# Performance work log

Measured on AMD Instinct MI355X. Metric: run time of the kernel, lower is better.

The kernel has to match this reference:

```python
import jax, jax.numpy as jnp
import numpy as np

B, H, Wd, CIN = 4, 64, 64, 65   # batch, height, width, in_channels (incl. time)
COUT = 256                      # out_channels (incl. time)
K = 3
KK = K * K
PAD, STRIDE = 1, 1
SOUT = 4                        # output_stabilizer_size (C4 rotations)
CURV = 1.0                      # Lorentz manifold curvature k
LIN_FEAT = (CIN - 1) * KK + 1   # 577


def make_c4_z2_indices(ksize):
    # (out_rotation, in_stabilizer=1, u, v, [s, u_src, v_src]) index table,
    # realizing the C4 filter rotation as a gather (as in GrouPy).
    f = np.arange(ksize * ksize).reshape(ksize, ksize)
    inds = np.zeros((4, 1, ksize, ksize, 3), dtype=np.int64)
    for r in range(4):
        rot = np.rot90(f, r)
        u, v = np.unravel_index(rot, (ksize, ksize))
        inds[r, 0, :, :, 1] = u
        inds[r, 0, :, :, 2] = v
    return inds

INDS = make_c4_z2_indices(K)


def setup_inputs() -> dict:
    key = jax.random.key(0)
    k1, k2, k3 = jax.random.split(key, 3)
    stdv = float(np.sqrt(2.0 / ((CIN - 1) * KK)))  # reset_parameters
    x = jax.random.normal(k1, (B, H, Wd, CIN), dtype=jnp.float32)
    W = jax.random.uniform(k2, (COUT, LIN_FEAT), minval=-stdv, maxval=stdv, dtype=jnp.float32)
    b = jax.random.uniform(k3, (COUT,), minval=-stdv, maxval=stdv, dtype=jnp.float32)
    return {"x": x, "W": W, "b": b}


def _unfold(x):
    # x: (B, C, H, W) -> (B, C*KK, Ho*Wo) in torch.nn.Unfold layout (channel-major, kernel-minor)
    xp = jnp.pad(x, ((0, 0), (0, 0), (PAD, PAD), (PAD, PAD)))
    ho = (H + 2 * PAD - K) // STRIDE + 1
    wo = (Wd + 2 * PAD - K) // STRIDE + 1
    cols = [xp[:, :, i:i + ho * STRIDE:STRIDE, j:j + wo * STRIDE:STRIDE]
            for i in range(K) for j in range(K)]
    p = jnp.stack(cols, axis=2)  # (B, C, KK, ho, wo)
    return p.reshape(B, CIN * KK, ho * wo), ho, wo


def _forward(x, W, b):
    # torch code does x.view(B, C, H, W) on channel-last data: a reshape, not a permute.
    xv = x.reshape(B, CIN, H, Wd)
    patches, ho, wo = _unfold(xv)
    patches = jnp.transpose(patches, (0, 2, 1))          # (B, P, C*KK)
    P = patches.shape[1]
    patches = patches.reshape(B, P, CIN, 1, K, K)
    patches = jnp.broadcast_to(patches, (B, P, CIN, SOUT, K, K))  # repeat over group dim
    # --- group-equivariant filter transform realized as a gather on patches ---
    ir = INDS.reshape(-1, 3)                              # (SOUT*KK, 3)
    pi = patches[:, :, :, ir[:, 0], ir[:, 1], ir[:, 2]]   # (B, P, C, SOUT*KK)
    pi = pi.reshape(B, P, CIN, SOUT, KK)
    pt = jnp.transpose(pi, (3, 0, 1, 2, 4)).reshape(SOUT, B, P, CIN * KK)
    # --- extract_lorentz_patches (vectorized over group dim) ---
    sqrt_k = jnp.sqrt(jnp.float32(CURV))
    t = jnp.maximum(pt[..., :KK], sqrt_k)                 # clamp time components
    t_resc = jnp.sqrt(jnp.sum(t * t, axis=-1, keepdims=True) - (KK - 1) * CURV)
    sp = pt[..., KK:]                                     # (SOUT,B,P,(C-1)*KK) channel-major
    sp = sp.reshape(SOUT, B, P, CIN - 1, KK).swapaxes(-1, -2).reshape(SOUT, B, P, (CIN - 1) * KK)
    pre = jnp.concatenate([t_resc, sp], axis=-1)          # (SOUT,B,P,LIN_FEAT)
    # --- LorentzFullyConnected: linear, then recompute time from space norm ---
    y = jnp.einsum('gbpf,of->gbpo', pre, W) + b           # (SOUT,B,P,COUT)
    y_sp = y[..., 1:]
    y_t = jnp.sqrt(jnp.sum(y_sp * y_sp, axis=-1, keepdims=True) + CURV)
    out = jnp.concatenate([y_t, y_sp], axis=-1)
    out = jnp.transpose(out, (1, 0, 2, 3)).reshape(B, SOUT, ho, wo, COUT)
    return out


def reference(x, W, b):
    return _forward(x, W, b)
```

## Files before the change

kernel.cpp:

```cpp
#include <hip/hip_runtime.h>
#include <hip/hip_bf16.h>

#define CIN 65
#define LIN 577
#define NSTEP 18
#define M_  16384

typedef __bf16 bf16x8 __attribute__((ext_vector_type(8)));
typedef float  f32x4  __attribute__((ext_vector_type(4)));
typedef unsigned short u16x8 __attribute__((ext_vector_type(8)));

__constant__ int SIG[4][9] = {
  {0,1,2,3,4,5,6,7,8},
  {2,5,8,1,4,7,0,3,6},
  {8,7,6,5,4,3,2,1,0},
  {6,3,0,7,4,1,8,5,2}};

__device__ __forceinline__ int swzm(int r) { return (r ^ (r >> 2)) & 3; }

__global__ __launch_bounds__(512) void prep_k(const float* __restrict__ x,
                                              const float* __restrict__ W,
                                              __hip_bfloat16* __restrict__ A,
                                              __hip_bfloat16* __restrict__ Wg,
                                              float* __restrict__ T) {
  __shared__ float lds[CIN * 3 * 72];
  const int tid = threadIdx.x;
  if (blockIdx.x >= 256) {
    int pidx = (blockIdx.x - 256) * 512 + tid;
    int jc  = pidx & 3;
    int col = (pidx >> 2) & 255;
    int t   = pidx >> 10;
    int ks  = t % NSTEP, g = t / NSTEP;
    int k   = SIG[(4 - g) & 3][ks >> 1];
    const float* src = W + col * LIN + 1 + k * 64 + (ks & 1) * 32 + jc * 8;
    u16x8 pk;
#pragma unroll
    for (int e = 0; e < 8; ++e) {
      union { __hip_bfloat16 h; unsigned short u; } cv;
      cv.h = __float2bfloat16(src[e]);
      pk[e] = cv.u;
    }
    *(u16x8*)(Wg + (size_t)pidx * 8) = pk;
    return;
  }
  const int b = blockIdx.x >> 6, py = blockIdx.x & 63;
  const float* xb = x + (size_t)b * (CIN * 4096);
  for (int i = tid; i < CIN * 3 * 18; i += 512)
    *(f32x4*)&lds[i * 4] = (f32x4){0.f, 0.f, 0.f, 0.f};
  __syncthreads();
  for (int i = tid; i < CIN * 3 * 16; i += 512) {
    int pr = i >> 4, j = i & 15;
    int c = pr / 3, dy = pr - c * 3;
    int hy = py + dy - 1;
    if (hy >= 0 && hy < 64)
      *(f32x4*)&lds[c * 216 + dy * 72 + 4 + j * 4] =
          *(const f32x4*)(xb + c * 4096 + hy * 64 + j * 4);
  }
  __syncthreads();

  const int wave = tid >> 6, px = tid & 63;
  const int rowid = (blockIdx.x << 6) | px;
#pragma unroll
  for (int qi = 0; qi < 9; ++qi) {
    int q = wave * 9 + qi;
    int m = q >> 3, cb8 = q & 7;
    int dy = m / 3, dx = m - dy * 3;
    const float* src = &lds[(1 + cb8 * 8) * 216 + dy * 72 + 3 + dx + px];
    u16x8 pk;
#pragma unroll
    for (int e = 0; e < 8; ++e) {
      union { __hip_bfloat16 h; unsigned short u; } cv;
      cv.h = __float2bfloat16(src[e * 216]);
      pk[e] = cv.u;
    }
    *(u16x8*)(A + ((size_t)q * M_ + rowid) * 8) = pk;
  }
  if (wave == 0) {
    float s = 0.f;
#pragma unroll
    for (int m = 0; m < 9; ++m) {
      float t = fmaxf(lds[(m / 3) * 72 + 3 + (m % 3) + px], 1.f);
      s += t * t;
    }
    T[rowid] = sqrtf(s - 8.f);
  }
}

__device__ __forceinline__ void async_cp16(const void* g, void* ldsbase) {
  __builtin_amdgcn_global_load_lds(
      (const __attribute__((address_space(1))) void*)g,
      (__attribute__((address_space(3))) void*)ldsbase, 16, 0, 0);
}

__global__ __launch_bounds__(512, 6) void gemm_k(const __hip_bfloat16* __restrict__ A,
                                                 const __hip_bfloat16* __restrict__ Wg,
                                                 const float* __restrict__ W,
                                                 const float* __restrict__ bias,
                                                 const float* __restrict__ T,
                                                 float* __restrict__ out) {
  __shared__ __align__(16) char smem[42240];
  const int fid = blockIdx.x;
  const int lid = ((fid & 7) << 7) | (fid >> 3);
  const int g = lid & 3, rb = lid >> 2;
  const int brow = rb << 6;
  const int tid = threadIdx.x, wave = tid >> 6, lane = tid & 63;
  const int fr = lane & 15, fq = lane >> 4;
  const int wr = (wave >> 2) * 32, wcb = (wave & 3) * 64;

  float* Tsh = (float*)(smem + 40960);
  float* Ps  = (float*)(smem + 41216);
  if (tid < 64) Tsh[tid] = T[brow + tid];

  const int arow = tid >> 2;
  const int alc  = (tid & 3) ^ swzm(arow);
  const int bc0  = tid >> 2, bl0 = (tid & 3) ^ swzm(bc0);
  const int bc1  = 128 + (tid >> 2), bl1 = (tid & 3) ^ swzm(bc1);
  const __hip_bfloat16* Wgg = Wg + ((size_t)(g * NSTEP) << 13);

  auto STAGE = [&](int buf, int ks) {
    if (tid < 256)
      async_cp16(A + (((size_t)(ks * 4 + alc) * M_ + brow + arow) << 3),
                 smem + buf * 4096 + wave * 1024);
    const __hip_bfloat16* bs = Wgg + ((size_t)ks << 13);
    char* bl = smem + 8192 + buf * 16384 + wave * 1024;
    async_cp16(bs + bc0 * 32 + bl0 * 8, bl);
    async_cp16(bs + bc1 * 32 + bl1 * 8, bl + 8192);
  };

  f32x4 acc[2][4] = {};
  auto COMPUTE = [&](int buf) {
    const char* Ab = smem + buf * 4096;
    const char* Bb = smem + 8192 + buf * 16384;
    bf16x8 af[2], bf[4];
#pragma unroll
    for (int i = 0; i < 2; ++i) {
      int r = wr + i * 16 + fr;
      af[i] = *(const bf16x8*)(Ab + r * 64 + ((fq ^ swzm(r)) << 4));
    }
#pragma unroll
    for (int j = 0; j < 4; ++j) {
      int c = wcb + j * 16 + fr;
      bf[j] = *(const bf16x8*)(Bb + c * 64 + ((fq ^ swzm(c)) << 4));
    }
    __builtin_amdgcn_s_setprio(1);
#pragma unroll
    for (int i = 0; i < 2; ++i)
#pragma unroll
      for (int j = 0; j < 4; ++j)
        acc[i][j] = __builtin_amdgcn_mfma_f32_16x16x32_bf16(af[i], bf[j], acc[i][j], 0, 0, 0);
    __builtin_amdgcn_s_setprio(0);
  };

  STAGE(0, 0);
  __syncthreads();
  for (int ks = 0; ks < NSTEP; ++ks) {
    if (ks + 1 < NSTEP) STAGE((ks + 1) & 1, ks + 1);
    COMPUTE(ks & 1);
    __syncthreads();
  }

  float bo[4], w0v[4]; int oc[4];
#pragma unroll
  for (int j = 0; j < 4; ++j) {
    oc[j]  = wcb + j * 16 + fr;
    bo[j]  = bias[oc[j]];
    w0v[j] = W[oc[j] * LIN];
  }
#pragma unroll
  for (int i = 0; i < 2; ++i) {
#pragma unroll
    for (int rr = 0; rr < 4; ++rr) {
      int rl = wr + i * 16 + fq * 4 + rr;
      int row = brow + rl;
      size_t obase = ((size_t)(((row >> 12) * 4 + g) * 4096 + (row & 4095)) << 8);
      float tval = Tsh[rl];
      float s = 0.f;
#pragma unroll
      for (int j = 0; j < 4; ++j) {
        float y = acc[i][j][rr] + bo[j] + tval * w0v[j];
        if (oc[j] != 0) { s += y * y; out[obase + oc[j]] = y; }
      }
      s += __shfl_xor(s, 1); s += __shfl_xor(s, 2);
      s += __shfl_xor(s, 4); s += __shfl_xor(s, 8);
      if (fr == 0) Ps[rl * 4 + (wave & 3)] = s;
    }
  }
  __syncthreads();
  if (tid < 64) {
    int row = brow + tid;
    float s = Ps[tid * 4] + Ps[tid * 4 + 1] + Ps[tid * 4 + 2] + Ps[tid * 4 + 3] + 1.0f;
    out[(size_t)(((row >> 12) * 4 + g) * 4096 + (row & 4095)) << 8] = sqrtf(s);
  }
}

extern "C" void kernel_launch(void* const* d_in, const int* in_sizes, int n_in,
                              void* d_out, int out_size, void* d_ws, size_t ws_size,
                              hipStream_t stream) {
  const float* x    = (const float*)d_in[0];
  const float* W    = (const float*)d_in[1];
  const float* bias = (const float*)d_in[2];
  float* out = (float*)d_out;

  char* ws = (char*)d_ws;
  __hip_bfloat16* Wg = (__hip_bfloat16*)ws;
  float*          T  = (float*)(ws + 1179648);
  __hip_bfloat16* A  = (__hip_bfloat16*)(ws + 1245184);

  prep_k<<<400, 512, 0, stream>>>(x, W, A, Wg, T);
  gemm_k<<<1024, 512, 0, stream>>>(A, Wg, W, bias, T, out);
}
```

Before: 50.10 us.

## Load GEMM fragments directly from global into registers, dropping LDS staging

Replaces the LDS double-buffered async global-to-LDS staging in the GEMM with direct per-lane global loads into register fragments, ping-ponged across two k-steps. It removes the per-step barriers and LDS traffic and shrinks shared memory to a small epilogue scratch. The cost is that operands shared between waves are now fetched redundantly from global/L2 rather than shared through LDS. The occupancy hint drops from 6 to 4 blocks to leave room for the extra live registers.

```diff
diff --git a/kernel.cpp b/kernel.cpp
--- a/kernel.cpp
+++ b/kernel.cpp
@@ -15,8 +15,6 @@
   {2,5,8,1,4,7,0,3,6},
   {8,7,6,5,4,3,2,1,0},
   {6,3,0,7,4,1,8,5,2}};
-
-__device__ __forceinline__ int swzm(int r) { return (r ^ (r >> 2)) & 3; }
 
 __global__ __launch_bounds__(512) void prep_k(const float* __restrict__ x,
                                               const float* __restrict__ W,
@@ -86,19 +84,13 @@
   }
 }
 
-__device__ __forceinline__ void async_cp16(const void* g, void* ldsbase) {
-  __builtin_amdgcn_global_load_lds(
-      (const __attribute__((address_space(1))) void*)g,
-      (__attribute__((address_space(3))) void*)ldsbase, 16, 0, 0);
-}
-
-__global__ __launch_bounds__(512, 6) void gemm_k(const __hip_bfloat16* __restrict__ A,
+__global__ __launch_bounds__(512, 4) void gemm_k(const __hip_bfloat16* __restrict__ A,
                                                  const __hip_bfloat16* __restrict__ Wg,
                                                  const float* __restrict__ W,
                                                  const float* __restrict__ bias,
                                                  const float* __restrict__ T,
                                                  float* __restrict__ out) {
-  __shared__ __align__(16) char smem[42240];
+  __shared__ __align__(16) char smem[1280];
   const int fid = blockIdx.x;
   const int lid = ((fid & 7) << 7) | (fid >> 3);
   const int g = lid & 3, rb = lid >> 2;
@@ -107,41 +99,26 @@
   const int fr = lane & 15, fq = lane >> 4;
   const int wr = (wave >> 2) * 32, wcb = (wave & 3) * 64;
 
-  float* Tsh = (float*)(smem + 40960);
-  float* Ps  = (float*)(smem + 41216);
+  float* Tsh = (float*)smem;
+  float* Ps  = (float*)(smem + 256);
   if (tid < 64) Tsh[tid] = T[brow + tid];
 
-  const int arow = tid >> 2;
-  const int alc  = (tid & 3) ^ swzm(arow);
-  const int bc0  = tid >> 2, bl0 = (tid & 3) ^ swzm(bc0);
-  const int bc1  = 128 + (tid >> 2), bl1 = (tid & 3) ^ swzm(bc1);
-  const __hip_bfloat16* Wgg = Wg + ((size_t)(g * NSTEP) << 13);
-
-  auto STAGE = [&](int buf, int ks) {
-    if (tid < 256)
-      async_cp16(A + (((size_t)(ks * 4 + alc) * M_ + brow + arow) << 3),
-                 smem + buf * 4096 + wave * 1024);
-    const __hip_bfloat16* bs = Wgg + ((size_t)ks << 13);
-    char* bl = smem + 8192 + buf * 16384 + wave * 1024;
-    async_cp16(bs + bc0 * 32 + bl0 * 8, bl);
-    async_cp16(bs + bc1 * 32 + bl1 * 8, bl + 8192);
+  const __hip_bfloat16* Aln = A + (((size_t)fq * M_ + brow + wr + fr) << 3);
+  auto LOADA = [&](bf16x8* dst, int ks) {
+#pragma unroll
+    for (int i = 0; i < 2; ++i)
+      dst[i] = *(const bf16x8*)(Aln + (size_t)ks * (M_ * 32) + i * 128);
+  };
+  const __hip_bfloat16* Bln = Wg + (((size_t)g * NSTEP) << 13)
+                                 + (size_t)(wcb + fr) * 32 + fq * 8;
+  auto LOADB = [&](bf16x8* dst, int ks) {
+#pragma unroll
+    for (int j = 0; j < 4; ++j)
+      dst[j] = *(const bf16x8*)(Bln + ((size_t)ks << 13) + j * 512);
   };
 
   f32x4 acc[2][4] = {};
-  auto COMPUTE = [&](int buf) {
-    const char* Ab = smem + buf * 4096;
-    const char* Bb = smem + 8192 + buf * 16384;
-    bf16x8 af[2], bf[4];
-#pragma unroll
-    for (int i = 0; i < 2; ++i) {
-      int r = wr + i * 16 + fr;
-      af[i] = *(const bf16x8*)(Ab + r * 64 + ((fq ^ swzm(r)) << 4));
-    }
-#pragma unroll
-    for (int j = 0; j < 4; ++j) {
-      int c = wcb + j * 16 + fr;
-      bf[j] = *(const bf16x8*)(Bb + c * 64 + ((fq ^ swzm(c)) << 4));
-    }
+  auto COMPUTE = [&](const bf16x8* af, const bf16x8* bf) {
     __builtin_amdgcn_s_setprio(1);
 #pragma unroll
     for (int i = 0; i < 2; ++i)
@@ -151,13 +128,15 @@
     __builtin_amdgcn_s_setprio(0);
   };
 
-  STAGE(0, 0);
+  bf16x8 afA[2], afB[2], bfA[4], bfB[4];
+  LOADA(afA, 0); LOADB(bfA, 0);
+  for (int kp = 0; kp < NSTEP; kp += 2) {
+    LOADA(afB, kp + 1); LOADB(bfB, kp + 1);
+    COMPUTE(afA, bfA);
+    if (kp + 2 < NSTEP) { LOADA(afA, kp + 2); LOADB(bfA, kp + 2); }
+    COMPUTE(afB, bfB);
+  }
   __syncthreads();
-  for (int ks = 0; ks < NSTEP; ++ks) {
-    if (ks + 1 < NSTEP) STAGE((ks + 1) & 1, ks + 1);
-    COMPUTE(ks & 1);
-    __syncthreads();
-  }
 
   float bo[4], w0v[4]; int oc[4];
 #pragma unroll
```

New measurement: 63.31 us. +26.4%, slower.
